# Kernel optimization log

Hardware: AMD Instinct MI355X
Metric: run time of the kernel (lower is better)

## Reference

```python
import jax, jax.numpy as jnp
import numpy as np

S = 3000    # number of candidate spans (rows of g_i)
P = 80000   # total (mention, antecedent) pairs
GI = 768    # gi_dim
DD = 20     # distance/genre/speaker embedding dim
HID = 150   # mlp hidden dim (fixed in source)
ORDER = 2   # N: one higher-order refinement pass


def setup_inputs() -> dict:
    key = jax.random.key(0)
    ks = jax.random.split(key, 18)
    gij = 3 * GI + 3 * DD
    g_i = jax.random.normal(ks[0], (S, GI), jnp.float32)
    mention_scores = jax.random.normal(ks[1], (S, 1), jnp.float32)
    # sorted segment ids: ragged antecedent counts per mention, grouped contiguously
    mention_ids = jnp.sort(jax.random.randint(ks[2], (P,), 0, S, dtype=jnp.int32))
    antecedent_ids = jax.random.randint(ks[3], (P,), 0, S, dtype=jnp.int32)
    dist_bins = jax.random.randint(ks[4], (P,), 0, 10, dtype=jnp.int32)
    genre_ids = jax.random.randint(ks[5], (P,), 0, 7, dtype=jnp.int32) + 1   # 1..7, 0 is padding_idx
    speaker_ids = jax.random.randint(ks[6], (P,), 0, 2, dtype=jnp.int32) + 1  # 1..2, 0 is padding_idx
    w = lambda k, shp: 0.02 * jax.random.normal(k, shp, jnp.float32)
    dist_emb = w(ks[7], (10, DD))
    genre_emb = w(ks[8], (8, DD)).at[0].set(0.0)     # padding_idx=0
    speaker_emb = w(ks[9], (3, DD)).at[0].set(0.0)   # padding_idx=0
    W1 = w(ks[10], (gij, HID)); b1 = jnp.zeros((HID,), jnp.float32)
    W2 = w(ks[11], (HID, HID)); b2 = jnp.zeros((HID,), jnp.float32)
    W3 = w(ks[12], (HID, 1)); b3 = jnp.zeros((1,), jnp.float32)
    Wf = w(ks[13], (2 * GI, 1)); bf = jnp.zeros((1,), jnp.float32)
    return {"g_i": g_i, "mention_scores": mention_scores, "mention_ids": mention_ids,
            "antecedent_ids": antecedent_ids, "dist_bins": dist_bins, "genre_ids": genre_ids,
            "speaker_ids": speaker_ids, "dist_emb": dist_emb, "genre_emb": genre_emb,
            "speaker_emb": speaker_emb, "W1": W1, "b1": b1, "W2": W2, "b2": b2,
            "W3": W3, "b3": b3, "Wf": Wf, "bf": bf}


def _mlp(x, W1, b1, W2, b2, W3, b3):
    h = jax.nn.relu(x @ W1 + b1)
    h = jax.nn.relu(h @ W2 + b2)
    return h @ W3 + b3


def reference(g_i, mention_scores, mention_ids, antecedent_ids, dist_bins, genre_ids,
              speaker_ids, dist_emb, genre_emb, speaker_emb, W1, b1, W2, b2, W3, b3, Wf, bf):
    phi = jnp.concatenate([dist_emb[dist_bins], genre_emb[genre_ids], speaker_emb[speaker_ids]], axis=1)  # [P,60]
    seg = dict(num_segments=S, indices_are_sorted=True)
    g = g_i
    scores = None
    for n in range(ORDER):
        i_g = g[mention_ids]                # [P,GI] gather
        j_g = g[antecedent_ids]             # [P,GI] gather
        pairs = jnp.concatenate([i_g, j_g, i_g * j_g, phi], axis=1)  # [P,gij]
        scores = _mlp(pairs, W1, b1, W2, b2, W3, b3)                 # [P,1]
        if n < ORDER - 1:
            # higher_order_refinement: ragged segment softmax + weighted scatter update
            s = scores[:, 0]
            seg_max = jax.ops.segment_max(s, mention_ids, **seg)
            safe_max = jnp.where(jnp.isfinite(seg_max), seg_max, 0.0)
            e = jnp.exp(s - safe_max[mention_ids])
            denom = jax.ops.segment_sum(e, mention_ids, **seg)
            attn = e / jnp.where(denom > 0, denom, 1.0)[mention_ids]
            weighted = jax.ops.segment_sum(attn[:, None] * j_g, mention_ids, **seg)  # [S,GI]
            counts = jax.ops.segment_sum(jnp.ones_like(s), mention_ids, **seg)
            f = jax.nn.sigmoid(jnp.concatenate([g, weighted], axis=1) @ Wf + bf)  # [S,1]
            # NOTE: faithful to the source bug: f * mention_id (the integer index), not f * mention_g
            ids_f = jnp.arange(S, dtype=g.dtype)[:, None]
            g_new = f * ids_f + (1.0 - f) * weighted
            g = jnp.where(counts[:, None] > 0, g_new, g)
    s_i = mention_scores[mention_ids]
    s_j = mention_scores[antecedent_ids]
    coref_scores = s_i + s_j + scores       # [P,1]
    # segment softmax with an extra epsilon (score 0) logit per mention
    c = coref_scores[:, 0]
    seg_max = jax.ops.segment_max(c, mention_ids, **seg)
    m = jnp.maximum(jnp.where(jnp.isfinite(seg_max), seg_max, 0.0), 0.0)  # include epsilon logit 0
    e = jnp.exp(c - m[mention_ids])
    denom = jax.ops.segment_sum(e, mention_ids, **seg) + jnp.exp(-m)
    pair_probs = e / denom[mention_ids]     # [P]
    eps_probs = jnp.exp(-m) / denom         # [S]
    return coref_scores, pair_probs, eps_probs
```

## Files before the change

kernel.cpp:

```cpp
#include <hip/hip_runtime.h>

#define GI   768
#define HID  150
#define HPAD 160
#define DDIM 20

typedef __attribute__((ext_vector_type(8))) short v8s;
typedef __attribute__((ext_vector_type(16))) float f32x16;

#define MFMA(A, B, C) __builtin_amdgcn_mfma_f32_32x32x16_bf16(A, B, C, 0, 0, 0)

__device__ __forceinline__ ushort bf16rn(float x) {
  unsigned u = __float_as_uint(x);
  return (ushort)((u + 0x7fffu + ((u >> 16) & 1u)) >> 16);
}
__device__ __forceinline__ void bsplit(float x, ushort& h, ushort& l) {
  h = bf16rn(x);
  float fh = __uint_as_float((unsigned)h << 16);
  l = bf16rn(x - fh);
}
__device__ __forceinline__ uint4 pack8(const ushort* v) {
  uint4 r;
  r.x = v[0] | ((unsigned)v[1] << 16); r.y = v[2] | ((unsigned)v[3] << 16);
  r.z = v[4] | ((unsigned)v[5] << 16); r.w = v[6] | ((unsigned)v[7] << 16);
  return r;
}

__device__ __forceinline__ int qoffb(int row, int kb) {
  return row * 96 + (kb ^ (((row >> 2) & 3) << 4));
}
__device__ __forceinline__ int hoffb(int row, int kb) {
  return row * 336 + (kb ^ (((row >> 3) & 3) << 4));
}

__global__ void seg_kernel(const int* __restrict__ mI, int* __restrict__ segs,
                           int P, int S) {
  int m = blockIdx.x * 256 + threadIdx.x;
  if (m > S) return;
  int lo = 0, hi = P;
  while (lo < hi) { int mid = (lo + hi) >> 1; if (mI[mid] < m) lo = mid + 1; else hi = mid; }
  segs[m] = lo;
}

__global__ void phi_kernel(const float* __restrict__ de, const float* __restrict__ ge,
                           const float* __restrict__ se, const float* __restrict__ W1,
                           float* __restrict__ phiW) {
  int idx = blockIdx.x * 256 + threadIdx.x;
  if (idx >= 21 * HPAD) return;
  int row = idx / HPAD, h = idx % HPAD;
  float v = 0.f;
  if (h < HID) {
    const float* emb; int off;
    if (row < 10)      { emb = de + row * DDIM;        off = 0; }
    else if (row < 18) { emb = ge + (row - 10) * DDIM; off = DDIM; }
    else               { emb = se + (row - 18) * DDIM; off = 2 * DDIM; }
    for (int k = 0; k < DDIM; ++k) v += emb[k] * W1[(3 * GI + off + k) * HID + h];
  }
  phiW[row * HPAD + h] = v;
}

__global__ void pad2_kernel(const float* __restrict__ W1, const float* __restrict__ W2,
                            const float* __restrict__ b1, const float* __restrict__ b2,
                            const float* __restrict__ W3,
                            ushort* __restrict__ WThi, ushort* __restrict__ WTlo,
                            ushort* __restrict__ W2Thi, ushort* __restrict__ W2Tlo,
                            float* __restrict__ b1p, float* __restrict__ b2p,
                            float* __restrict__ W3p) {
  int idx = blockIdx.x * 256 + threadIdx.x;
  if (idx < 480 * GI) {
    int c = idx / GI, r = idx % GI;
    int seg = c / HPAD, h = c % HPAD;
    float x = (h < HID) ? W1[(size_t)(seg * GI + r) * HID + h] : 0.f;
    ushort hh, ll; bsplit(x, hh, ll);
    WThi[idx] = hh; WTlo[idx] = ll; return;
  }
  idx -= 480 * GI;
  if (idx < HPAD * HPAD) {
    int c = idx / HPAD, k = idx % HPAD;
    float x = (c < HID && k < HID) ? W2[(size_t)k * HID + c] : 0.f;
    ushort hh, ll; bsplit(x, hh, ll);
    W2Thi[idx] = hh; W2Tlo[idx] = ll; return;
  }
  idx -= HPAD * HPAD;
  if (idx < HPAD) { b1p[idx] = (idx < HID) ? b1[idx] : 0.f; return; }
  idx -= HPAD;
  if (idx < HPAD) { b2p[idx] = (idx < HID) ? b2[idx] : 0.f; return; }
  idx -= HPAD;
  if (idx < HPAD) { W3p[idx] = (idx < HID) ? W3[idx] : 0.f; return; }
}

__global__ __launch_bounds__(320, 4) void pre2_kernel(
    const float* __restrict__ g, const ushort* __restrict__ WThi,
    const ushort* __restrict__ WTlo, float* __restrict__ pre, int S) {
  __shared__ char pool[12288];
  ushort* qhi = (ushort*)pool;
  ushort* qlo = qhi + 64 * 48;
  const int t = threadIdx.x;
  const int lane = t & 63, w = t >> 6;
  const int lcol = lane & 31, half = lane >> 5;
  const int row0 = blockIdx.x * 64;
  const int hb = blockIdx.y * HPAD;

  f32x16 acc0 = {}, acc1 = {};
  const ushort* wh = WThi + (size_t)(hb + w * 32 + lcol) * GI + 8 * half;
  const ushort* wl = WTlo + (size_t)(hb + w * 32 + lcol) * GI + 8 * half;

  const int qr = (t < 256) ? (t >> 2) : 0;
  const int kq = (t & 3) * 8;
  int srow = row0 + qr; if (srow >= S) srow = S - 1;
  const float* gp = g + (size_t)srow * GI + kq;
  char* qdH = (char*)qhi + qoffb(qr, kq * 2);
  char* qdL = (char*)qlo + qoffb(qr, kq * 2);

  for (int d0 = 0; d0 < GI; d0 += 32) {
    if (d0) __syncthreads();
    if (t < 256) {
      float4 a0 = *(const float4*)(gp + d0), a1 = *(const float4*)(gp + d0 + 4);
      float xr[8] = {a0.x, a0.y, a0.z, a0.w, a1.x, a1.y, a1.z, a1.w};
      ushort hs[8], ls[8];
#pragma unroll
      for (int j = 0; j < 8; ++j) bsplit(xr[j], hs[j], ls[j]);
      *(uint4*)qdH = pack8(hs); *(uint4*)qdL = pack8(ls);
    }
    __syncthreads();
#pragma unroll
    for (int kh = 0; kh < 2; ++kh) {
      v8s bh = *(const v8s*)(wh + d0 + 16 * kh);
      v8s bl = *(const v8s*)(wl + d0 + 16 * kh);
      const int kb = 32 * kh + 16 * half;
      v8s a0h = *(const v8s*)((char*)qhi + qoffb(lcol, kb));
      v8s a0l = *(const v8s*)((char*)qlo + qoffb(lcol, kb));
      acc0 = MFMA(a0h, bh, acc0); acc0 = MFMA(a0l, bh, acc0); acc0 = MFMA(a0h, bl, acc0);
      v8s a1h = *(const v8s*)((char*)qhi + qoffb(32 + lcol, kb));
      v8s a1l = *(const v8s*)((char*)qlo + qoffb(32 + lcol, kb));
      acc1 = MFMA(a1h, bh, acc1); acc1 = MFMA(a1l, bh, acc1); acc1 = MFMA(a1h, bl, acc1);
    }
  }
  const int h = w * 32 + lcol;
#pragma unroll
  for (int q = 0; q < 16; ++q) {
    int p = (q & 3) + 8 * (q >> 2) + 4 * half;
    int s0 = row0 + p;
    if (s0 < S) pre[(size_t)s0 * 320 + hb + h] = acc0[q];
    int s1 = row0 + 32 + p;
    if (s1 < S) pre[(size_t)s1 * 320 + hb + h] = acc1[q];
  }
}

__global__ __launch_bounds__(320, 4) void h1s_kernel(
    const float* __restrict__ g, const float* __restrict__ pre,
    const float* __restrict__ phiW,
    const ushort* __restrict__ WThi, const ushort* __restrict__ WTlo,
    const ushort* __restrict__ W2Thi, const ushort* __restrict__ W2Tlo,
    const float* __restrict__ b1p, const float* __restrict__ b2p,
    const float* __restrict__ W3p, const float* __restrict__ b3,
    const int* __restrict__ mI, const int* __restrict__ aI,
    const int* __restrict__ db, const int* __restrict__ ge, const int* __restrict__ sp,
    float* __restrict__ sOut, int P) {
  __shared__ char pool[43008];
  __shared__ int sIi[64], sIj[64], sRd[64], sRg[64], sRs[64];
  __shared__ float sRed[64];
  ushort* qhi = (ushort*)pool;
  ushort* qlo = qhi + 64 * 48;
  ushort* thi = (ushort*)pool;
  ushort* tlo = thi + 64 * 168;

  const int t = threadIdx.x;
  const int lane = t & 63, w = t >> 6;
  const int lcol = lane & 31, half = lane >> 5;
  const int p0 = blockIdx.x * 64;

  if (t < 64) {
    int p = p0 + t;
    sIi[t] = mI[p]; sIj[t] = aI[p];
    sRd[t] = db[p]; sRg[t] = 10 + ge[p]; sRs[t] = 18 + sp[p];
    sRed[t] = 0.f;
  }

  f32x16 acc0 = {}, acc1 = {};
  const ushort* wh = WThi + (size_t)(320 + w * 32 + lcol) * GI + 8 * half;
  const ushort* wl = WTlo + (size_t)(320 + w * 32 + lcol) * GI + 8 * half;

  __syncthreads();

  const int qr = (t < 256) ? (t >> 2) : 0;
  const int kq = (t & 3) * 8;
  const float* gi = g + (size_t)sIi[qr] * GI + kq;
  const float* gj = g + (size_t)sIj[qr] * GI + kq;
  char* qdH = (char*)qhi + qoffb(qr, kq * 2);
  char* qdL = (char*)qlo + qoffb(qr, kq * 2);

  for (int d0 = 0; d0 < GI; d0 += 32) {
    if (d0) __syncthreads();
    if (t < 256) {
      float4 a0 = *(const float4*)(gi + d0), a1 = *(const float4*)(gi + d0 + 4);
      float4 b0 = *(const float4*)(gj + d0), b1v = *(const float4*)(gj + d0 + 4);
      float xr[8] = {a0.x * b0.x, a0.y * b0.y, a0.z * b0.z, a0.w * b0.w,
                     a1.x * b1v.x, a1.y * b1v.y, a1.z * b1v.z, a1.w * b1v.w};
      ushort hs[8], ls[8];
#pragma unroll
      for (int j = 0; j < 8; ++j) bsplit(xr[j], hs[j], ls[j]);
      *(uint4*)qdH = pack8(hs); *(uint4*)qdL = pack8(ls);
    }
    __syncthreads();
#pragma unroll
    for (int kh = 0; kh < 2; ++kh) {
      v8s bh = *(const v8s*)(wh + d0 + 16 * kh);
      v8s bl = *(const v8s*)(wl + d0 + 16 * kh);
      const int kb = 32 * kh + 16 * half;
      v8s a0h = *(const v8s*)((char*)qhi + qoffb(lcol, kb));
      v8s a0l = *(const v8s*)((char*)qlo + qoffb(lcol, kb));
      acc0 = MFMA(a0h, bh, acc0); acc0 = MFMA(a0l, bh, acc0); acc0 = MFMA(a0h, bl, acc0);
      v8s a1h = *(const v8s*)((char*)qhi + qoffb(32 + lcol, kb));
      v8s a1l = *(const v8s*)((char*)qlo + qoffb(32 + lcol, kb));
      acc1 = MFMA(a1h, bh, acc1); acc1 = MFMA(a1l, bh, acc1); acc1 = MFMA(a1h, bl, acc1);
    }
  }
  __syncthreads();

  const int h = w * 32 + lcol;
  const float b1v = b1p[h];
#pragma unroll
  for (int q = 0; q < 16; ++q) {
    const int rr = (q & 3) + 8 * (q >> 2) + 4 * half;
    {
      int p = rr;
      float v = acc0[q] + b1v
              + pre[(size_t)sIi[p] * 320 + h] + pre[(size_t)sIj[p] * 320 + 160 + h]
              + phiW[sRd[p] * HPAD + h] + phiW[sRg[p] * HPAD + h] + phiW[sRs[p] * HPAD + h];
      v = fmaxf(v, 0.f);
      ushort hh, ll; bsplit(v, hh, ll);
      *(ushort*)((char*)thi + hoffb(p, 2 * h)) = hh;
      *(ushort*)((char*)tlo + hoffb(p, 2 * h)) = ll;
    }
    {
      int p = 32 + rr;
      float v = acc1[q] + b1v
              + pre[(size_t)sIi[p] * 320 + h] + pre[(size_t)sIj[p] * 320 + 160 + h]
              + phiW[sRd[p] * HPAD + h] + phiW[sRg[p] * HPAD + h] + phiW[sRs[p] * HPAD + h];
      v = fmaxf(v, 0.f);
      ushort hh, ll; bsplit(v, hh, ll);
      *(ushort*)((char*)thi + hoffb(p, 2 * h)) = hh;
      *(ushort*)((char*)tlo + hoffb(p, 2 * h)) = ll;
    }
  }
  __syncthreads();

  f32x16 c0 = {}, c1 = {};
  const ushort* u2h = W2Thi + (size_t)(w * 32 + lcol) * HPAD + 8 * half;
  const ushort* u2l = W2Tlo + (size_t)(w * 32 + lcol) * HPAD + 8 * half;
#pragma unroll
  for (int c = 0; c < HPAD; c += 32) {
#pragma unroll
    for (int kh = 0; kh < 2; ++kh) {
      v8s bh = *(const v8s*)(u2h + c + 16 * kh);
      v8s bl = *(const v8s*)(u2l + c + 16 * kh);
      const int kb = 2 * (c + 16 * kh) + 16 * half;
      v8s a0h = *(const v8s*)((char*)thi + hoffb(lcol, kb));
      v8s a0l = *(const v8s*)((char*)tlo + hoffb(lcol, kb));
      c0 = MFMA(a0h, bh, c0); c0 = MFMA(a0l, bh, c0); c0 = MFMA(a0h, bl, c0);
      v8s a1h = *(const v8s*)((char*)thi + hoffb(32 + lcol, kb));
      v8s a1l = *(const v8s*)((char*)tlo + hoffb(32 + lcol, kb));
      c1 = MFMA(a1h, bh, c1); c1 = MFMA(a1l, bh, c1); c1 = MFMA(a1h, bl, c1);
    }
  }

  const float b2v = b2p[h], w3v = W3p[h];
#pragma unroll
  for (int q = 0; q < 16; ++q) {
    float v0 = fmaxf(c0[q] + b2v, 0.f) * w3v;
    float v1 = fmaxf(c1[q] + b2v, 0.f) * w3v;
#pragma unroll
    for (int m = 16; m; m >>= 1) {
      v0 += __shfl_xor(v0, m, 32);
      v1 += __shfl_xor(v1, m, 32);
    }
    if (lcol == 0) {
      const int rr = (q & 3) + 8 * (q >> 2) + 4 * half;
      atomicAdd(&sRed[rr], v0);
      atomicAdd(&sRed[32 + rr], v1);
    }
  }
  __syncthreads();
  if (t < 64) sOut[p0 + t] = sRed[t] + b3[0];
}

__global__ void mid_kernel(const float* __restrict__ g, const float* __restrict__ s1,
                           const int* __restrict__ segs, const int* __restrict__ aI,
                           const float* __restrict__ Wf, const float* __restrict__ bf,
                           float* __restrict__ g2) {
  const int m = blockIdx.x;
  const int t = threadIdx.x;
  const int st = segs[m], en = segs[m + 1], n = en - st;
  if (n == 0) {
    for (int d = t; d < GI; d += 256) g2[m * GI + d] = g[m * GI + d];
    return;
  }
  __shared__ float red[256];
  float mx = -INFINITY;
  for (int p = st + t; p < en; p += 256) mx = fmaxf(mx, s1[p]);
  red[t] = mx; __syncthreads();
  for (int s = 128; s > 0; s >>= 1) { if (t < s) red[t] = fmaxf(red[t], red[t + s]); __syncthreads(); }
  mx = red[0]; __syncthreads();
  float sm = 0.f;
  for (int p = st + t; p < en; p += 256) sm += expf(s1[p] - mx);
  red[t] = sm; __syncthreads();
  for (int s = 128; s > 0; s >>= 1) { if (t < s) red[t] += red[t + s]; __syncthreads(); }
  const float denom = red[0]; __syncthreads();
  float wv[3] = {0.f, 0.f, 0.f};
  for (int p = st; p < en; ++p) {
    float e = expf(s1[p] - mx);
    const float* gj = g + (size_t)aI[p] * GI;
#pragma unroll
    for (int u = 0; u < 3; ++u) wv[u] += e * gj[t + u * 256];
  }
#pragma unroll
  for (int u = 0; u < 3; ++u) wv[u] /= denom;
  float part = 0.f;
#pragma unroll
  for (int u = 0; u < 3; ++u) {
    int d = t + u * 256;
    part += g[m * GI + d] * Wf[d] + wv[u] * Wf[GI + d];
  }
  red[t] = part; __syncthreads();
  for (int s = 128; s > 0; s >>= 1) { if (t < s) red[t] += red[t + s]; __syncthreads(); }
  const float f = 1.f / (1.f + expf(-(red[0] + bf[0])));
#pragma unroll
  for (int u = 0; u < 3; ++u) {
    int d = t + u * 256;
    g2[m * GI + d] = f * (float)m + (1.f - f) * wv[u];
  }
}

__global__ void coref_kernel(const float* __restrict__ ms, const float* __restrict__ s2,
                             const int* __restrict__ mI, const int* __restrict__ aI,
                             float* __restrict__ out, int P) {
  int p = blockIdx.x * 256 + threadIdx.x;
  if (p >= P) return;
  out[p] = ms[mI[p]] + ms[aI[p]] + s2[p];
}

__global__ void final_kernel(const float* __restrict__ c, const int* __restrict__ segs,
                             float* __restrict__ pairP, float* __restrict__ epsP) {
  const int m = blockIdx.x;
  const int t = threadIdx.x;
  const int st = segs[m], en = segs[m + 1], n = en - st;
  __shared__ float red[256];
  float mx = -INFINITY;
  for (int p = st + t; p < en; p += 256) mx = fmaxf(mx, c[p]);
  red[t] = mx; __syncthreads();
  for (int s = 128; s > 0; s >>= 1) { if (t < s) red[t] = fmaxf(red[t], red[t + s]); __syncthreads(); }
  mx = red[0]; __syncthreads();
  const float m2 = (n > 0) ? fmaxf(mx, 0.f) : 0.f;
  float sm = 0.f;
  for (int p = st + t; p < en; p += 256) sm += expf(c[p] - m2);
  red[t] = sm; __syncthreads();
  for (int s = 128; s > 0; s >>= 1) { if (t < s) red[t] += red[t + s]; __syncthreads(); }
  const float denom = red[0] + expf(-m2);
  for (int p = st + t; p < en; p += 256) pairP[p] = expf(c[p] - m2) / denom;
  if (t == 0) epsP[m] = expf(-m2) / denom;
}

extern "C" void kernel_launch(void* const* d_in, const int* in_sizes, int n_in,
                              void* d_out, int out_size, void* d_ws, size_t ws_size,
                              hipStream_t stream) {
  const float* g_i  = (const float*)d_in[0];
  const float* ms   = (const float*)d_in[1];
  const int*   mI   = (const int*)d_in[2];
  const int*   aI   = (const int*)d_in[3];
  const int*   db   = (const int*)d_in[4];
  const int*   ge   = (const int*)d_in[5];
  const int*   sp   = (const int*)d_in[6];
  const float* de   = (const float*)d_in[7];
  const float* gemb = (const float*)d_in[8];
  const float* semb = (const float*)d_in[9];
  const float* W1   = (const float*)d_in[10];
  const float* b1   = (const float*)d_in[11];
  const float* W2   = (const float*)d_in[12];
  const float* b2   = (const float*)d_in[13];
  const float* W3   = (const float*)d_in[14];
  const float* b3   = (const float*)d_in[15];
  const float* Wf   = (const float*)d_in[16];
  const float* bf   = (const float*)d_in[17];

  const int S = in_sizes[0] / GI;
  const int P = in_sizes[2];
  float* out = (float*)d_out;

  char* ws = (char*)d_ws;
  size_t off = 0;
  auto take = [&](size_t bytes) -> char* {
    char* p = ws + off;
    off = (off + bytes + 15) & ~(size_t)15;
    return p;
  };
  int*    segs  = (int*)   take((size_t)(S + 1) * 4);
  float*  phiW  = (float*) take((size_t)21 * HPAD * 4);
  float*  pre   = (float*) take((size_t)S * 320 * 4);
  float*  g2    = (float*) take((size_t)S * GI * 4);
  float*  s1    = (float*) take((size_t)P * 4);
  float*  s2    = (float*) take((size_t)P * 4);
  ushort* WThi  = (ushort*)take((size_t)480 * GI * 2);
  ushort* WTlo  = (ushort*)take((size_t)480 * GI * 2);
  ushort* W2Thi = (ushort*)take((size_t)HPAD * HPAD * 2);
  ushort* W2Tlo = (ushort*)take((size_t)HPAD * HPAD * 2);
  float*  b1p   = (float*) take((size_t)HPAD * 4);
  float*  b2p   = (float*) take((size_t)HPAD * 4);
  float*  W3p   = (float*) take((size_t)HPAD * 4);

  const int gridSeg = (S + 1 + 255) / 256;
  const int gridPhi = (21 * HPAD + 255) / 256;
  const int gridPad = (480 * GI + HPAD * HPAD + 3 * HPAD + 255) / 256;
  const dim3 gridPre((S + 63) / 64, 2);
  const int gridH   = P / 64;
  const int gridCor = (P + 255) / 256;

  seg_kernel<<<gridSeg, 256, 0, stream>>>(mI, segs, P, S);
  phi_kernel<<<gridPhi, 256, 0, stream>>>(de, gemb, semb, W1, phiW);
  pad2_kernel<<<gridPad, 256, 0, stream>>>(W1, W2, b1, b2, W3,
                                           WThi, WTlo, W2Thi, W2Tlo, b1p, b2p, W3p);

  pre2_kernel<<<gridPre, 320, 0, stream>>>(g_i, WThi, WTlo, pre, S);
  h1s_kernel<<<gridH, 320, 0, stream>>>(g_i, pre, phiW, WThi, WTlo, W2Thi, W2Tlo,
                                        b1p, b2p, W3p, b3, mI, aI, db, ge, sp, s1, P);
  mid_kernel<<<S, 256, 0, stream>>>(g_i, s1, segs, aI, Wf, bf, g2);

  pre2_kernel<<<gridPre, 320, 0, stream>>>(g2, WThi, WTlo, pre, S);
  h1s_kernel<<<gridH, 320, 0, stream>>>(g2, pre, phiW, WThi, WTlo, W2Thi, W2Tlo,
                                        b1p, b2p, W3p, b3, mI, aI, db, ge, sp, s2, P);

  coref_kernel<<<gridCor, 256, 0, stream>>>(ms, s2, mI, aI, out, P);
  final_kernel<<<S, 256, 0, stream>>>(out, segs, out + P, out + 2 * (size_t)P);
}
```

Measured before the change: 495.5 us.

## Double-buffer LDS tiles and prefetch next K-chunk in GEMM loops

Both the pre2 and h1s kernels now use two LDS buffers. Each loop iteration issues global loads for the next 32-wide K chunk of g (or the g_i*g_j product) and of the weights before running the MFMAs on the current buffer. The bf16 split of the prefetched data is written to the other buffer after the MFMAs, so only one barrier is needed per iteration instead of two. This hides global load latency behind matrix math, at the cost of double the LDS footprint in pre2 and more registers held for the prefetched values.

```diff
diff --git a/kernel.cpp b/kernel.cpp
--- a/kernel.cpp
+++ b/kernel.cpp
@@ -92,9 +92,7 @@
 __global__ __launch_bounds__(320, 4) void pre2_kernel(
     const float* __restrict__ g, const ushort* __restrict__ WThi,
     const ushort* __restrict__ WTlo, float* __restrict__ pre, int S) {
-  __shared__ char pool[12288];
-  ushort* qhi = (ushort*)pool;
-  ushort* qlo = qhi + 64 * 48;
+  __shared__ char pool[24576];
   const int t = threadIdx.x;
   const int lane = t & 63, w = t >> 6;
   const int lcol = lane & 31, half = lane >> 5;
@@ -106,36 +104,67 @@
   const ushort* wl = WTlo + (size_t)(hb + w * 32 + lcol) * GI + 8 * half;
 
   const int qr = (t < 256) ? (t >> 2) : 0;
-  const int kq = (t & 3) * 8;
+  const int qob = qoffb(qr, (t & 3) * 16);
   int srow = row0 + qr; if (srow >= S) srow = S - 1;
-  const float* gp = g + (size_t)srow * GI + kq;
-  char* qdH = (char*)qhi + qoffb(qr, kq * 2);
-  char* qdL = (char*)qlo + qoffb(qr, kq * 2);
-
+  const float* gp = g + (size_t)srow * GI + (t & 3) * 8;
+
+  if (t < 256) {
+    float4 a0 = *(const float4*)(gp), a1 = *(const float4*)(gp + 4);
+    float xr[8] = {a0.x, a0.y, a0.z, a0.w, a1.x, a1.y, a1.z, a1.w};
+    ushort hs[8], ls[8];
+#pragma unroll
+    for (int j = 0; j < 8; ++j) bsplit(xr[j], hs[j], ls[j]);
+    *(uint4*)(pool + qob) = pack8(hs);
+    *(uint4*)(pool + 6144 + qob) = pack8(ls);
+  }
+  v8s cwh0 = *(const v8s*)(wh), cwh1 = *(const v8s*)(wh + 16);
+  v8s cwl0 = *(const v8s*)(wl), cwl1 = *(const v8s*)(wl + 16);
+  __syncthreads();
+
+  int cur = 0;
+#pragma unroll 1
   for (int d0 = 0; d0 < GI; d0 += 32) {
-    if (d0) __syncthreads();
-    if (t < 256) {
-      float4 a0 = *(const float4*)(gp + d0), a1 = *(const float4*)(gp + d0 + 4);
-      float xr[8] = {a0.x, a0.y, a0.z, a0.w, a1.x, a1.y, a1.z, a1.w};
+    const bool has = (d0 + 32) < GI;
+    const int dn = has ? d0 + 32 : 0;
+    float4 na0, na1;
+    if (t < 256) { na0 = *(const float4*)(gp + dn); na1 = *(const float4*)(gp + dn + 4); }
+    v8s nwh0 = *(const v8s*)(wh + dn), nwh1 = *(const v8s*)(wh + dn + 16);
+    v8s nwl0 = *(const v8s*)(wl + dn), nwl1 = *(const v8s*)(wl + dn + 16);
+
+    const char* qh = pool + cur * 12288;
+    const char* ql = qh + 6144;
+    {
+      const int kb = 16 * half;
+      v8s a0h = *(const v8s*)(qh + qoffb(lcol, kb));
+      v8s a0l = *(const v8s*)(ql + qoffb(lcol, kb));
+      acc0 = MFMA(a0h, cwh0, acc0); acc0 = MFMA(a0l, cwh0, acc0); acc0 = MFMA(a0h, cwl0, acc0);
+      v8s a1h = *(const v8s*)(qh + qoffb(32 + lcol, kb));
+      v8s a1l = *(const v8s*)(ql + qoffb(32 + lcol, kb));
+      acc1 = MFMA(a1h, cwh0, acc1); acc1 = MFMA(a1l, cwh0, acc1); acc1 = MFMA(a1h, cwl0, acc1);
+    }
+    {
+      const int kb = 32 + 16 * half;
+      v8s a0h = *(const v8s*)(qh + qoffb(lcol, kb));
+      v8s a0l = *(const v8s*)(ql + qoffb(lcol, kb));
+      acc0 = MFMA(a0h, cwh1, acc0); acc0 = MFMA(a0l, cwh1, acc0); acc0 = MFMA(a0h, cwl1, acc0);
+      v8s a1h = *(const v8s*)(qh + qoffb(32 + lcol, kb));
+      v8s a1l = *(const v8s*)(ql + qoffb(32 + lcol, kb));
+      acc1 = MFMA(a1h, cwh1, acc1); acc1 = MFMA(a1l, cwh1, acc1); acc1 = MFMA(a1h, cwl1, acc1);
+    }
+    if (has && t < 256) {
+      float xr[8] = {na0.x, na0.y, na0.z, na0.w, na1.x, na1.y, na1.z, na1.w};
       ushort hs[8], ls[8];
 #pragma unroll
       for (int j = 0; j < 8; ++j) bsplit(xr[j], hs[j], ls[j]);
-      *(uint4*)qdH = pack8(hs); *(uint4*)qdL = pack8(ls);
-    }
+      char* dst = pool + (cur ^ 1) * 12288;
+      *(uint4*)(dst + qob) = pack8(hs);
+      *(uint4*)(dst + 6144 + qob) = pack8(ls);
+    }
+    cwh0 = nwh0; cwh1 = nwh1; cwl0 = nwl0; cwl1 = nwl1;
     __syncthreads();
-#pragma unroll
-    for (int kh = 0; kh < 2; ++kh) {
-      v8s bh = *(const v8s*)(wh + d0 + 16 * kh);
-      v8s bl = *(const v8s*)(wl + d0 + 16 * kh);
-      const int kb = 32 * kh + 16 * half;
-      v8s a0h = *(const v8s*)((char*)qhi + qoffb(lcol, kb));
-      v8s a0l = *(const v8s*)((char*)qlo + qoffb(lcol, kb));
-      acc0 = MFMA(a0h, bh, acc0); acc0 = MFMA(a0l, bh, acc0); acc0 = MFMA(a0h, bl, acc0);
-      v8s a1h = *(const v8s*)((char*)qhi + qoffb(32 + lcol, kb));
-      v8s a1l = *(const v8s*)((char*)qlo + qoffb(32 + lcol, kb));
-      acc1 = MFMA(a1h, bh, acc1); acc1 = MFMA(a1l, bh, acc1); acc1 = MFMA(a1h, bl, acc1);
-    }
-  }
+    cur ^= 1;
+  }
+
   const int h = w * 32 + lcol;
 #pragma unroll
   for (int q = 0; q < 16; ++q) {
@@ -160,8 +189,6 @@
   __shared__ char pool[43008];
   __shared__ int sIi[64], sIj[64], sRd[64], sRg[64], sRs[64];
   __shared__ float sRed[64];
-  ushort* qhi = (ushort*)pool;
-  ushort* qlo = qhi + 64 * 48;
   ushort* thi = (ushort*)pool;
   ushort* tlo = thi + 64 * 168;
 
@@ -184,39 +211,72 @@
   __syncthreads();
 
   const int qr = (t < 256) ? (t >> 2) : 0;
-  const int kq = (t & 3) * 8;
-  const float* gi = g + (size_t)sIi[qr] * GI + kq;
-  const float* gj = g + (size_t)sIj[qr] * GI + kq;
-  char* qdH = (char*)qhi + qoffb(qr, kq * 2);
-  char* qdL = (char*)qlo + qoffb(qr, kq * 2);
-
+  const int qob = qoffb(qr, (t & 3) * 16);
+  const float* gi = g + (size_t)sIi[qr] * GI + (t & 3) * 8;
+  const float* gj = g + (size_t)sIj[qr] * GI + (t & 3) * 8;
+
+  if (t < 256) {
+    float4 a0 = *(const float4*)(gi), a1 = *(const float4*)(gi + 4);
+    float4 b0 = *(const float4*)(gj), b1v = *(const float4*)(gj + 4);
+    float xr[8] = {a0.x * b0.x, a0.y * b0.y, a0.z * b0.z, a0.w * b0.w,
+                   a1.x * b1v.x, a1.y * b1v.y, a1.z * b1v.z, a1.w * b1v.w};
+    ushort hs[8], ls[8];
+#pragma unroll
+    for (int j = 0; j < 8; ++j) bsplit(xr[j], hs[j], ls[j]);
+    *(uint4*)(pool + qob) = pack8(hs);
+    *(uint4*)(pool + 6144 + qob) = pack8(ls);
+  }
+  v8s cwh0 = *(const v8s*)(wh), cwh1 = *(const v8s*)(wh + 16);
+  v8s cwl0 = *(const v8s*)(wl), cwl1 = *(const v8s*)(wl + 16);
+  __syncthreads();
+
+  int cur = 0;
+#pragma unroll 1
   for (int d0 = 0; d0 < GI; d0 += 32) {
-    if (d0) __syncthreads();
+    const bool has = (d0 + 32) < GI;
+    const int dn = has ? d0 + 32 : 0;
+    float4 na0, na1, nb0, nb1;
     if (t < 256) {
-      float4 a0 = *(const float4*)(gi + d0), a1 = *(const float4*)(gi + d0 + 4);
-      float4 b0 = *(const float4*)(gj + d0), b1v = *(const float4*)(gj + d0 + 4);
-      float xr[8] = {a0.x * b0.x, a0.y * b0.y, a0.z * b0.z, a0.w * b0.w,
-                     a1.x * b1v.x, a1.y * b1v.y, a1.z * b1v.z, a1.w * b1v.w};
+      na0 = *(const float4*)(gi + dn); na1 = *(const float4*)(gi + dn + 4);
+      nb0 = *(const float4*)(gj + dn); nb1 = *(const float4*)(gj + dn + 4);
+    }
+    v8s nwh0 = *(const v8s*)(wh + dn), nwh1 = *(const v8s*)(wh + dn + 16);
+    v8s nwl0 = *(const v8s*)(wl + dn), nwl1 = *(const v8s*)(wl + dn + 16);
+
+    const char* qh = pool + cur * 12288;
+    const char* ql = qh + 6144;
+    {
+      const int kb = 16 * half;
+      v8s a0h = *(const v8s*)(qh + qoffb(lcol, kb));
+      v8s a0l = *(const v8s*)(ql + qoffb(lcol, kb));
+      acc0 = MFMA(a0h, cwh0, acc0); acc0 = MFMA(a0l, cwh0, acc0); acc0 = MFMA(a0h, cwl0, acc0);
+      v8s a1h = *(const v8s*)(qh + qoffb(32 + lcol, kb));
+      v8s a1l = *(const v8s*)(ql + qoffb(32 + lcol, kb));
+      acc1 = MFMA(a1h, cwh0, acc1); acc1 = MFMA(a1l, cwh0, acc1); acc1 = MFMA(a1h, cwl0, acc1);
+    }
+    {
+      const int kb = 32 + 16 * half;
+      v8s a0h = *(const v8s*)(qh + qoffb(lcol, kb));
+      v8s a0l = *(const v8s*)(ql + qoffb(lcol, kb));
+      acc0 = MFMA(a0h, cwh1, acc0); acc0 = MFMA(a0l, cwh1, acc0); acc0 = MFMA(a0h, cwl1, acc0);
+      v8s a1h = *(const v8s*)(qh + qoffb(32 + lcol, kb));
+      v8s a1l = *(const v8s*)(ql + qoffb(32 + lcol, kb));
+      acc1 = MFMA(a1h, cwh1, acc1); acc1 = MFMA(a1l, cwh1, acc1); acc1 = MFMA(a1h, cwl1, acc1);
+    }
+    if (has && t < 256) {
+      float xr[8] = {na0.x * nb0.x, na0.y * nb0.y, na0.z * nb0.z, na0.w * nb0.w,
+                     na1.x * nb1.x, na1.y * nb1.y, na1.z * nb1.z, na1.w * nb1.w};
       ushort hs[8], ls[8];
 #pragma unroll
       for (int j = 0; j < 8; ++j) bsplit(xr[j], hs[j], ls[j]);
-      *(uint4*)qdH = pack8(hs); *(uint4*)qdL = pack8(ls);
-    }
+      char* dst = pool + (cur ^ 1) * 12288;
+      *(uint4*)(dst + qob) = pack8(hs);
+      *(uint4*)(dst + 6144 + qob) = pack8(ls);
+    }
+    cwh0 = nwh0; cwh1 = nwh1; cwl0 = nwl0; cwl1 = nwl1;
     __syncthreads();
-#pragma unroll
-    for (int kh = 0; kh < 2; ++kh) {
-      v8s bh = *(const v8s*)(wh + d0 + 16 * kh);
-      v8s bl = *(const v8s*)(wl + d0 + 16 * kh);
-      const int kb = 32 * kh + 16 * half;
-      v8s a0h = *(const v8s*)((char*)qhi + qoffb(lcol, kb));
-      v8s a0l = *(const v8s*)((char*)qlo + qoffb(lcol, kb));
-      acc0 = MFMA(a0h, bh, acc0); acc0 = MFMA(a0l, bh, acc0); acc0 = MFMA(a0h, bl, acc0);
-      v8s a1h = *(const v8s*)((char*)qhi + qoffb(32 + lcol, kb));
-      v8s a1l = *(const v8s*)((char*)qlo + qoffb(32 + lcol, kb));
-      acc1 = MFMA(a1h, bh, acc1); acc1 = MFMA(a1l, bh, acc1); acc1 = MFMA(a1h, bl, acc1);
-    }
-  }
-  __syncthreads();
+    cur ^= 1;
+  }
 
   const int h = w * 32 + lcol;
   const float b1v = b1p[h];
```

Result: faster. 449.2 us (-9.4%).
